# Performance work log

Measured on AMD Instinct MI355X. Metric: run time of the kernel, lower is better.

Reference implementation:

```python
import jax, jax.numpy as jnp
import numpy as np

HEAD = 8
LN_EPS = 1e-5


def setup_inputs() -> dict:
    key = jax.random.key(0)
    k1, k2, k3, k4 = jax.random.split(key, 4)
    B, N, C = 1, 4096, 128
    x = jax.random.normal(k1, (B, N, C), dtype=jnp.float32)
    A = jax.random.normal(k2, (B, N, HEAD, 1), dtype=jnp.float32)
    # xavier-ish scaled params
    W_qk = jax.random.normal(k3, (C, 2 * C), dtype=jnp.float32) * (1.0 / np.sqrt(C))
    W_v = jax.random.normal(k4, (1, 1), dtype=jnp.float32)
    ln_g = jnp.ones((C,), dtype=jnp.float32)
    ln_b = jnp.zeros((C,), dtype=jnp.float32)
    return {"x": x, "A": A, "W_qk": W_qk, "W_v": W_v, "ln_g": ln_g, "ln_b": ln_b}


def _layernorm(x, g, b):
    mu = jnp.mean(x, axis=-1, keepdims=True)
    var = jnp.mean(jnp.square(x - mu), axis=-1, keepdims=True)
    return (x - mu) * jax.lax.rsqrt(var + LN_EPS) * g + b


def reference(x, A, W_qk, W_v, ln_g, ln_b):
    B, N, C = x.shape
    hd = C // HEAD
    scale = C ** (-0.5)  # NOTE: full dim, as in original (dim ** -0.5)
    xn = _layernorm(x, ln_g, ln_b)
    qk = (xn @ W_qk).reshape(B, N, 2, HEAD, hd)
    q = jnp.transpose(qk[:, :, 0], (0, 2, 1, 3))  # [B,H,N,hd]
    k = jnp.transpose(qk[:, :, 1], (0, 2, 1, 3))  # [B,H,N,hd]
    v = A * W_v[0, 0]                              # Linear(1,1,bias=False)
    v = jnp.transpose(v, (0, 2, 1, 3))             # [B,H,N,1]
    scores = jnp.einsum("bhnd,bhmd->bhnm", q, k) * scale
    attn = jax.nn.softmax(scores, axis=-1)
    out = jnp.einsum("bhnm,bhmv->bhnv", attn, v)   # [B,H,N,1]
    A_plus = jnp.transpose(out, (0, 2, 1, 3))      # [B,N,H,1]
    return A + A_plus
```

## Files before the change

kernel.cpp:

```cpp
#include <hip/hip_runtime.h>

#define HEADS 8
#define NTOK 4096
#define CH 128
#define KSPLIT 8
#define KCHUNK (NTOK / KSPLIT)
#define LN_EPS 1e-5f

typedef short short8 __attribute__((ext_vector_type(8)));
typedef float f32x4 __attribute__((ext_vector_type(4)));
typedef float f32x2 __attribute__((ext_vector_type(2)));
typedef float f32x16 __attribute__((ext_vector_type(16)));

__device__ inline unsigned short f2bf(float f) {
    unsigned int u = __float_as_uint(f);
    u = (u + 0x7FFFu + ((u >> 16) & 1u)) >> 16;
    return (unsigned short)u;
}

__device__ inline float fast_exp2(float x) {
#if __has_builtin(__builtin_amdgcn_exp2f)
    return __builtin_amdgcn_exp2f(x);
#else
    float r; asm volatile("v_exp_f32 %0, %1" : "=v"(r) : "v"(x)); return r;
#endif
}

__device__ inline f32x2 fma2(f32x2 a, f32x2 b, f32x2 c) {
#if __has_builtin(__builtin_elementwise_fma)
    return __builtin_elementwise_fma(a, b, c);
#else
    f32x2 r; r.x = fmaf(a.x, b.x, c.x); r.y = fmaf(a.y, b.y, c.y); return r;
#endif
}

#define SC (0.08838834764831845f * 1.4426950408889634f)

__global__ __launch_bounds__(256) void ln_qk_fused(
    const float* __restrict__ x, const float* __restrict__ Wqk,
    const float* __restrict__ g, const float* __restrict__ b,
    const float* __restrict__ A,
    unsigned short* __restrict__ qb, unsigned short* __restrict__ kbuf,
    float* __restrict__ vT)
{
    __shared__ __align__(16) unsigned short xn_s[16][CH];
    const int tid = threadIdx.x;
    const int wave = tid >> 6, lane = tid & 63;
    const int row0 = blockIdx.x * 16;
    const int ct = blockIdx.y * 4 + wave;
    const int j = lane & 15, grp = lane >> 4;

    const float sc = (ct < 8) ? SC : 1.0f;
    short8 wf[4];
    #pragma unroll
    for (int ks = 0; ks < 4; ++ks) {
        unsigned int uu0, uu1, uu2, uu3;
        const float* wp = Wqk + (ks * 32 + grp * 8) * 256 + ct * 16 + j;
        uu0 = f2bf(wp[0 * 256] * sc) | ((unsigned)f2bf(wp[1 * 256] * sc) << 16);
        uu1 = f2bf(wp[2 * 256] * sc) | ((unsigned)f2bf(wp[3 * 256] * sc) << 16);
        uu2 = f2bf(wp[4 * 256] * sc) | ((unsigned)f2bf(wp[5 * 256] * sc) << 16);
        uu3 = f2bf(wp[6 * 256] * sc) | ((unsigned)f2bf(wp[7 * 256] * sc) << 16);
        uint4 packed = {uu0, uu1, uu2, uu3};
        wf[ks] = *(short8*)&packed;
    }

    if (blockIdx.y == 0 && tid < 128) {
        const int hh = tid >> 4, r = tid & 15;
        vT[hh * NTOK + row0 + r] = A[(size_t)(row0 + r) * HEADS + hh];
    }

    for (int rr = wave; rr < 16; rr += 4) {
        const int row = row0 + rr;
        float2 xv = *(const float2*)(x + row * CH + lane * 2);
        float s  = xv.x + xv.y;
        float sq = xv.x * xv.x + xv.y * xv.y;
        #pragma unroll
        for (int off = 32; off >= 1; off >>= 1) {
            s  += __shfl_xor(s, off);
            sq += __shfl_xor(sq, off);
        }
        float mu  = s * (1.0f / CH);
        float var = sq * (1.0f / CH) - mu * mu;
        float rs  = rsqrtf(var + LN_EPS);
        float2 gv = *(const float2*)(g + lane * 2);
        float2 bv = *(const float2*)(b + lane * 2);
        unsigned int lo = f2bf((xv.x - mu) * rs * gv.x + bv.x);
        unsigned int hi = f2bf((xv.y - mu) * rs * gv.y + bv.y);
        const int c = (lane * 2) ^ ((rr & 7) << 3);
        *(unsigned int*)&xn_s[rr][c] = lo | (hi << 16);
    }
    __syncthreads();

    short8 af[4];
    #pragma unroll
    for (int ks = 0; ks < 4; ++ks)
        af[ks] = *(const short8*)(&xn_s[j][(ks * 32 + grp * 8) ^ ((j & 7) << 3)]);

    f32x4 acc = {0.f, 0.f, 0.f, 0.f};
    #pragma unroll
    for (int ks = 0; ks < 4; ++ks)
        acc = __builtin_amdgcn_mfma_f32_16x16x32_bf16(af[ks], wf[ks], acc, 0, 0, 0);

    unsigned short* dst = (ct < 8)
        ? qb   + ((size_t)ct * NTOK + row0) * 16
        : kbuf + ((size_t)(ct - 8) * NTOK + row0) * 16;
    #pragma unroll
    for (int r = 0; r < 4; ++r)
        dst[(grp * 4 + r) * 16 + j] = f2bf(acc[r]);
}

__global__ __launch_bounds__(256) void attn_kernel(
    const unsigned short* __restrict__ qb, const unsigned short* __restrict__ kbuf,
    const float* __restrict__ vT,
    float* __restrict__ partE, float* __restrict__ partF)
{
    const int tid = threadIdx.x;
    const int wave = tid >> 6, lane = tid & 63;
    const int ksp = blockIdx.y, h = blockIdx.z;
    const int q0 = blockIdx.x * 128 + wave * 32;
    const int m0 = ksp * KCHUNK;
    const int c  = lane & 31;
    const int hi = lane >> 5;

    short8 qf = *(const short8*)(qb + ((size_t)(h * NTOK + q0 + c) * 16 + hi * 8));

    const unsigned short* kl = kbuf + ((size_t)(h * NTOK + m0 + c) * 16 + hi * 8);
    const float* vl = vT + h * NTOK + m0 + hi * 4;

    f32x2 E2 = {0.f, 0.f}, F2 = {0.f, 0.f};
    short8 kf = *(const short8*)kl;

    for (int mi = 0; mi < KCHUNK; mi += 32) {
        const int nx = (mi + 32 < KCHUNK) ? mi + 32 : 0;
        short8 kn = *(const short8*)(kl + (size_t)nx * 16);

        f32x4 v0 = *(const f32x4*)(vl + mi);
        f32x4 v1 = *(const f32x4*)(vl + mi + 8);
        f32x4 v2 = *(const f32x4*)(vl + mi + 16);
        f32x4 v3 = *(const f32x4*)(vl + mi + 24);

        f32x16 z = {0.f};
        f32x16 s = __builtin_amdgcn_mfma_f32_32x32x16_bf16(kf, qf, z, 0, 0, 0);

        #pragma unroll
        for (int gg = 0; gg < 4; ++gg) {
            f32x4 vg = (gg == 0) ? v0 : (gg == 1) ? v1 : (gg == 2) ? v2 : v3;
            f32x2 pa, pb;
            pa.x = fast_exp2(s[gg * 4 + 0]);
            pa.y = fast_exp2(s[gg * 4 + 1]);
            pb.x = fast_exp2(s[gg * 4 + 2]);
            pb.y = fast_exp2(s[gg * 4 + 3]);
            E2 += pa;
            E2 += pb;
            F2 = fma2(pa, vg.xy, F2);
            F2 = fma2(pb, vg.zw, F2);
        }
        kf = kn;
    }

    float e = E2.x + E2.y;
    float f = F2.x + F2.y;
    e += __shfl_xor(e, 32);
    f += __shfl_xor(f, 32);

    if (lane < 32) {
        const int base = (ksp * HEADS + h) * NTOK;
        partE[base + q0 + c] = e;
        partF[base + q0 + c] = f;
    }
}

__global__ __launch_bounds__(256) void reduce_kernel(
    const float* __restrict__ partE, const float* __restrict__ partF,
    const float* __restrict__ A, const float* __restrict__ Wv,
    float* __restrict__ out)
{
    const int t = blockIdx.x * 256 + threadIdx.x;
    const int n = t >> 3;
    const int h = t & 7;
    float E = 0.f, F = 0.f;
    #pragma unroll
    for (int s = 0; s < KSPLIT; ++s) {
        E += partE[(s * HEADS + h) * NTOK + n];
        F += partF[(s * HEADS + h) * NTOK + n];
    }
    out[t] = A[t] + Wv[0] * F / E;
}

extern "C" void kernel_launch(void* const* d_in, const int* in_sizes, int n_in,
                              void* d_out, int out_size, void* d_ws, size_t ws_size,
                              hipStream_t stream)
{
    const float* x   = (const float*)d_in[0];
    const float* A   = (const float*)d_in[1];
    const float* Wqk = (const float*)d_in[2];
    const float* Wv  = (const float*)d_in[3];
    const float* g   = (const float*)d_in[4];
    const float* b   = (const float*)d_in[5];
    float* out = (float*)d_out;

    float* partE = (float*)d_ws;
    float* partF = partE + KSPLIT * HEADS * NTOK;
    unsigned short* qb   = (unsigned short*)(partF + KSPLIT * HEADS * NTOK);
    unsigned short* kbuf = qb + (size_t)HEADS * NTOK * 16;
    float* vT = (float*)(kbuf + (size_t)HEADS * NTOK * 16);

    ln_qk_fused<<<dim3(NTOK / 16, 4), dim3(256), 0, stream>>>(
        x, Wqk, g, b, A, qb, kbuf, vT);
    attn_kernel<<<dim3(NTOK / 128, KSPLIT, HEADS), dim3(256), 0, stream>>>(
        qb, kbuf, vT, partE, partF);
    reduce_kernel<<<dim3(NTOK * HEADS / 256), dim3(256), 0, stream>>>(
        partE, partF, A, Wv, out);
}
```

Measured before the change: 35.57 us.

## Fuse split-K reduction into attention kernel via last-block atomic counter

```diff
diff --git a/kernel.cpp b/kernel.cpp
--- a/kernel.cpp
+++ b/kernel.cpp
@@ -5,6 +5,8 @@
 #define CH 128
 #define KSPLIT 8
 #define KCHUNK (NTOK / KSPLIT)
+#define QTILE 128
+#define NQT (NTOK / QTILE)
 #define LN_EPS 1e-5f
 
 typedef short short8 __attribute__((ext_vector_type(8)));
@@ -41,7 +43,7 @@
     const float* __restrict__ g, const float* __restrict__ b,
     const float* __restrict__ A,
     unsigned short* __restrict__ qb, unsigned short* __restrict__ kbuf,
-    float* __restrict__ vT)
+    float* __restrict__ vT, unsigned int* __restrict__ cnt)
 {
     __shared__ __align__(16) unsigned short xn_s[16][CH];
     const int tid = threadIdx.x;
@@ -49,6 +51,9 @@
     const int row0 = blockIdx.x * 16;
     const int ct = blockIdx.y * 4 + wave;
     const int j = lane & 15, grp = lane >> 4;
+
+    if (blockIdx.x == 0 && blockIdx.y == 0)
+        cnt[tid] = 0;
 
     const float sc = (ct < 8) ? SC : 1.0f;
     short8 wf[4];
@@ -111,13 +116,15 @@
 
 __global__ __launch_bounds__(256) void attn_kernel(
     const unsigned short* __restrict__ qb, const unsigned short* __restrict__ kbuf,
-    const float* __restrict__ vT,
-    float* __restrict__ partE, float* __restrict__ partF)
+    const float* __restrict__ vT, const float* __restrict__ A,
+    const float* __restrict__ Wv,
+    float* __restrict__ partE, float* __restrict__ partF,
+    unsigned int* __restrict__ cnt, float* __restrict__ out)
 {
     const int tid = threadIdx.x;
     const int wave = tid >> 6, lane = tid & 63;
-    const int ksp = blockIdx.y, h = blockIdx.z;
-    const int q0 = blockIdx.x * 128 + wave * 32;
+    const int qt = blockIdx.x, ksp = blockIdx.y, h = blockIdx.z;
+    const int q0 = qt * QTILE + wave * 32;
     const int m0 = ksp * KCHUNK;
     const int c  = lane & 31;
     const int hi = lane >> 5;
@@ -163,28 +170,35 @@
     e += __shfl_xor(e, 32);
     f += __shfl_xor(f, 32);
 
+    const int slot = (qt * HEADS + h) * KSPLIT + ksp;
     if (lane < 32) {
-        const int base = (ksp * HEADS + h) * NTOK;
-        partE[base + q0 + c] = e;
-        partF[base + q0 + c] = f;
-    }
-}
-
-__global__ __launch_bounds__(256) void reduce_kernel(
-    const float* __restrict__ partE, const float* __restrict__ partF,
-    const float* __restrict__ A, const float* __restrict__ Wv,
-    float* __restrict__ out)
-{
-    const int t = blockIdx.x * 256 + threadIdx.x;
-    const int n = t >> 3;
-    const int h = t & 7;
-    float E = 0.f, F = 0.f;
-    #pragma unroll
-    for (int s = 0; s < KSPLIT; ++s) {
-        E += partE[(s * HEADS + h) * NTOK + n];
-        F += partF[(s * HEADS + h) * NTOK + n];
-    }
-    out[t] = A[t] + Wv[0] * F / E;
+        partE[slot * QTILE + wave * 32 + c] = e;
+        partF[slot * QTILE + wave * 32 + c] = f;
+    }
+
+    __shared__ bool last_s;
+    __syncthreads();
+    if (tid == 0) {
+        __threadfence();
+        unsigned int old = atomicAdd(&cnt[qt * HEADS + h], 1u);
+        last_s = (old == KSPLIT - 1);
+    }
+    __syncthreads();
+    if (!last_s) return;
+    __threadfence();
+
+    if (tid < QTILE) {
+        const int q = qt * QTILE + tid;
+        const float* pe = partE + (size_t)(qt * HEADS + h) * KSPLIT * QTILE + tid;
+        const float* pf = partF + (size_t)(qt * HEADS + h) * KSPLIT * QTILE + tid;
+        float E = 0.f, F = 0.f;
+        #pragma unroll
+        for (int s = 0; s < KSPLIT; ++s) {
+            E += pe[s * QTILE];
+            F += pf[s * QTILE];
+        }
+        out[q * HEADS + h] = A[q * HEADS + h] + Wv[0] * F / E;
+    }
 }
 
 extern "C" void kernel_launch(void* const* d_in, const int* in_sizes, int n_in,
@@ -200,15 +214,14 @@
     float* out = (float*)d_out;
 
     float* partE = (float*)d_ws;
-    float* partF = partE + KSPLIT * HEADS * NTOK;
-    unsigned short* qb   = (unsigned short*)(partF + KSPLIT * HEADS * NTOK);
+    float* partF = partE + (size_t)NQT * HEADS * KSPLIT * QTILE;
+    unsigned short* qb   = (unsigned short*)(partF + (size_t)NQT * HEADS * KSPLIT * QTILE);
     unsigned short* kbuf = qb + (size_t)HEADS * NTOK * 16;
     float* vT = (float*)(kbuf + (size_t)HEADS * NTOK * 16);
+    unsigned int* cnt = (unsigned int*)(vT + (size_t)HEADS * NTOK);
 
     ln_qk_fused<<<dim3(NTOK / 16, 4), dim3(256), 0, stream>>>(
-        x, Wqk, g, b, A, qb, kbuf, vT);
-    attn_kernel<<<dim3(NTOK / 128, KSPLIT, HEADS), dim3(256), 0, stream>>>(
-        qb, kbuf, vT, partE, partF);
-    reduce_kernel<<<dim3(NTOK * HEADS / 256), dim3(256), 0, stream>>>(
-        partE, partF, A, Wv, out);
-}
+        x, Wqk, g, b, A, qb, kbuf, vT, cnt);
+    attn_kernel<<<dim3(NQT, KSPLIT, HEADS), dim3(256), 0, stream>>>(
+        qb, kbuf, vT, A, Wv, partE, partF, cnt, out);
+}
```

Measured after the change: 90.65 us. 2.55x slower.

## Halve key split and regroup partial sums by query tile and head

Applied to the files above, without the earlier changes.

```diff
diff --git a/kernel.cpp b/kernel.cpp
--- a/kernel.cpp
+++ b/kernel.cpp
@@ -3,8 +3,10 @@
 #define HEADS 8
 #define NTOK 4096
 #define CH 128
-#define KSPLIT 8
+#define KSPLIT 4
 #define KCHUNK (NTOK / KSPLIT)
+#define QTILE 128
+#define NQT (NTOK / QTILE)
 #define LN_EPS 1e-5f
 
 typedef short short8 __attribute__((ext_vector_type(8)));
@@ -116,8 +118,8 @@
 {
     const int tid = threadIdx.x;
     const int wave = tid >> 6, lane = tid & 63;
-    const int ksp = blockIdx.y, h = blockIdx.z;
-    const int q0 = blockIdx.x * 128 + wave * 32;
+    const int qt = blockIdx.x, ksp = blockIdx.y, h = blockIdx.z;
+    const int q0 = qt * QTILE + wave * 32;
     const int m0 = ksp * KCHUNK;
     const int c  = lane & 31;
     const int hi = lane >> 5;
@@ -164,9 +166,9 @@
     f += __shfl_xor(f, 32);
 
     if (lane < 32) {
-        const int base = (ksp * HEADS + h) * NTOK;
-        partE[base + q0 + c] = e;
-        partF[base + q0 + c] = f;
+        const size_t slot = ((size_t)(qt * HEADS + h) * KSPLIT + ksp) * QTILE;
+        partE[slot + wave * 32 + c] = e;
+        partF[slot + wave * 32 + c] = f;
     }
 }
 
@@ -176,15 +178,19 @@
     float* __restrict__ out)
 {
     const int t = blockIdx.x * 256 + threadIdx.x;
-    const int n = t >> 3;
-    const int h = t & 7;
+    const int pair = t >> 7;
+    const int i = t & (QTILE - 1);
+    const int q = (pair >> 3) * QTILE + i;
+    const int h = pair & 7;
+    const float* pe = partE + (size_t)pair * KSPLIT * QTILE + i;
+    const float* pf = partF + (size_t)pair * KSPLIT * QTILE + i;
     float E = 0.f, F = 0.f;
     #pragma unroll
     for (int s = 0; s < KSPLIT; ++s) {
-        E += partE[(s * HEADS + h) * NTOK + n];
-        F += partF[(s * HEADS + h) * NTOK + n];
-    }
-    out[t] = A[t] + Wv[0] * F / E;
+        E += pe[s * QTILE];
+        F += pf[s * QTILE];
+    }
+    out[q * HEADS + h] = A[q * HEADS + h] + Wv[0] * F / E;
 }
 
 extern "C" void kernel_launch(void* const* d_in, const int* in_sizes, int n_in,
@@ -200,14 +206,14 @@
     float* out = (float*)d_out;
 
     float* partE = (float*)d_ws;
-    float* partF = partE + KSPLIT * HEADS * NTOK;
-    unsigned short* qb   = (unsigned short*)(partF + KSPLIT * HEADS * NTOK);
+    float* partF = partE + (size_t)NQT * HEADS * KSPLIT * QTILE;
+    unsigned short* qb   = (unsigned short*)(partF + (size_t)NQT * HEADS * KSPLIT * QTILE);
     unsigned short* kbuf = qb + (size_t)HEADS * NTOK * 16;
     float* vT = (float*)(kbuf + (size_t)HEADS * NTOK * 16);
 
     ln_qk_fused<<<dim3(NTOK / 16, 4), dim3(256), 0, stream>>>(
         x, Wqk, g, b, A, qb, kbuf, vT);
-    attn_kernel<<<dim3(NTOK / 128, KSPLIT, HEADS), dim3(256), 0, stream>>>(
+    attn_kernel<<<dim3(NQT, KSPLIT, HEADS), dim3(256), 0, stream>>>(
         qb, kbuf, vT, partE, partF);
     reduce_kernel<<<dim3(NTOK * HEADS / 256), dim3(256), 0, stream>>>(
         partE, partF, A, Wv, out);
```

Result: faster. 34.68 us (-2.5%).

## Fuse split-K reduction into attention kernel via shared memory

Applied to the files above, without the earlier changes.

```diff
diff --git a/kernel.cpp b/kernel.cpp
--- a/kernel.cpp
+++ b/kernel.cpp
@@ -3,7 +3,7 @@
 #define HEADS 8
 #define NTOK 4096
 #define CH 128
-#define KSPLIT 8
+#define KSPLIT 4
 #define KCHUNK (NTOK / KSPLIT)
 #define LN_EPS 1e-5f
 
@@ -109,15 +109,16 @@
         dst[(grp * 4 + r) * 16 + j] = f2bf(acc[r]);
 }
 
-__global__ __launch_bounds__(256) void attn_kernel(
+__global__ __launch_bounds__(512, 4) void attn_kernel(
     const unsigned short* __restrict__ qb, const unsigned short* __restrict__ kbuf,
-    const float* __restrict__ vT,
-    float* __restrict__ partE, float* __restrict__ partF)
+    const float* __restrict__ vT, const float* __restrict__ A,
+    const float* __restrict__ Wv, float* __restrict__ out)
 {
     const int tid = threadIdx.x;
     const int wave = tid >> 6, lane = tid & 63;
-    const int ksp = blockIdx.y, h = blockIdx.z;
-    const int q0 = blockIdx.x * 128 + wave * 32;
+    const int qt = blockIdx.x, h = blockIdx.y;
+    const int qw = wave & 1, ksp = wave >> 1;
+    const int q0 = qt * 64 + qw * 32;
     const int m0 = ksp * KCHUNK;
     const int c  = lane & 31;
     const int hi = lane >> 5;
@@ -163,28 +164,25 @@
     e += __shfl_xor(e, 32);
     f += __shfl_xor(f, 32);
 
+    __shared__ float eb[2][KSPLIT][32];
+    __shared__ float fb[2][KSPLIT][32];
     if (lane < 32) {
-        const int base = (ksp * HEADS + h) * NTOK;
-        partE[base + q0 + c] = e;
-        partF[base + q0 + c] = f;
-    }
-}
-
-__global__ __launch_bounds__(256) void reduce_kernel(
-    const float* __restrict__ partE, const float* __restrict__ partF,
-    const float* __restrict__ A, const float* __restrict__ Wv,
-    float* __restrict__ out)
-{
-    const int t = blockIdx.x * 256 + threadIdx.x;
-    const int n = t >> 3;
-    const int h = t & 7;
-    float E = 0.f, F = 0.f;
-    #pragma unroll
-    for (int s = 0; s < KSPLIT; ++s) {
-        E += partE[(s * HEADS + h) * NTOK + n];
-        F += partF[(s * HEADS + h) * NTOK + n];
-    }
-    out[t] = A[t] + Wv[0] * F / E;
+        eb[qw][ksp][c] = e;
+        fb[qw][ksp][c] = f;
+    }
+    __syncthreads();
+
+    if (tid < 64) {
+        const int qw2 = tid >> 5, c2 = tid & 31;
+        float E = eb[qw2][0][c2], F = fb[qw2][0][c2];
+        #pragma unroll
+        for (int s = 1; s < KSPLIT; ++s) {
+            E += eb[qw2][s][c2];
+            F += fb[qw2][s][c2];
+        }
+        const int q = qt * 64 + qw2 * 32 + c2;
+        out[q * HEADS + h] = A[q * HEADS + h] + Wv[0] * F / E;
+    }
 }
 
 extern "C" void kernel_launch(void* const* d_in, const int* in_sizes, int n_in,
@@ -199,16 +197,12 @@
     const float* b   = (const float*)d_in[5];
     float* out = (float*)d_out;
 
-    float* partE = (float*)d_ws;
-    float* partF = partE + KSPLIT * HEADS * NTOK;
-    unsigned short* qb   = (unsigned short*)(partF + KSPLIT * HEADS * NTOK);
+    unsigned short* qb   = (unsigned short*)d_ws;
     unsigned short* kbuf = qb + (size_t)HEADS * NTOK * 16;
     float* vT = (float*)(kbuf + (size_t)HEADS * NTOK * 16);
 
     ln_qk_fused<<<dim3(NTOK / 16, 4), dim3(256), 0, stream>>>(
         x, Wqk, g, b, A, qb, kbuf, vT);
-    attn_kernel<<<dim3(NTOK / 128, KSPLIT, HEADS), dim3(256), 0, stream>>>(
-        qb, kbuf, vT, partE, partF);
-    reduce_kernel<<<dim3(NTOK * HEADS / 256), dim3(256), 0, stream>>>(
-        partE, partF, A, Wv, out);
-}
+    attn_kernel<<<dim3(NTOK / 64, HEADS), dim3(512), 0, stream>>>(
+        qb, kbuf, vT, A, Wv, out);
+}
```

Result: faster. 33.28 us (-6.4%).
